# Performance work log

Measured on AMD Instinct MI355X. Metric: run time of the kernel, lower is better.

## Reference

```python
import jax, jax.numpy as jnp
import numpy as np

D_IN = 6      # raw node feature dim (self_attn_init first arg)
D_INIT = 16   # init encoding dim (self_attn_init second arg)
D_CAT = 22    # 6 + 16 (self_attn_enc first arg)
D_ENC = 64    # encoding dim (self_attn_enc second arg / gated_aggr_attn)
N = 1024      # number of nodes in node_cloud


def setup_inputs() -> dict:
    key = jax.random.key(0)
    ks = jax.random.split(key, 8)
    return {
        "node_cloud": jax.random.normal(ks[0], (N, D_IN), jnp.float32),
        "Wq_i": jax.random.normal(ks[1], (D_IN, D_INIT), jnp.float32) / np.sqrt(D_IN),
        "Wk_i": jax.random.normal(ks[2], (D_IN, D_INIT), jnp.float32) / np.sqrt(D_IN),
        "Wv_i": jax.random.normal(ks[3], (D_IN, D_INIT), jnp.float32) / np.sqrt(D_IN),
        "Wq_e": jax.random.normal(ks[4], (D_IN, D_ENC), jnp.float32) / np.sqrt(D_IN),
        "Wk_e": jax.random.normal(ks[5], (D_CAT, D_ENC), jnp.float32) / np.sqrt(D_CAT),
        "Wv_e": jax.random.normal(ks[6], (D_CAT, D_ENC), jnp.float32) / np.sqrt(D_CAT),
        "wg": jax.random.normal(ks[7], (D_ENC,), jnp.float32) / np.sqrt(D_ENC),
        "bg": jnp.zeros((), jnp.float32),
    }


def reference(node_cloud, Wq_i, Wk_i, Wv_i, Wq_e, Wk_e, Wv_e, wg, bg):
    # Stage 1: self_attn_init, batched over all C=N centres at once.
    # Per centre c: attend over every node, per-node 16-d encoding.
    Q_i = node_cloud @ Wq_i                     # [C, 16] (one query per centre)
    K_i = node_cloud @ Wk_i                     # [N, 16]
    V_i = node_cloud @ Wv_i                     # [N, 16]
    scores_i = (Q_i @ K_i.T) / np.sqrt(D_INIT)  # [C, N]
    a_i = jax.nn.softmax(scores_i, axis=-1)     # [C, N]
    nce_init = a_i[:, :, None] * V_i[None]      # [C, N, 16]

    # Stage 2: self_attn_enc on concat(raw node feats, init encodings).
    x = jnp.concatenate(
        [jnp.broadcast_to(node_cloud[None], (N, N, D_IN)), nce_init], axis=-1
    )                                            # [C, N, 22]
    Q_e = node_cloud @ Wq_e                      # [C, 64]
    K_e = jnp.einsum("cnf,fd->cnd", x, Wk_e)     # [C, N, 64]
    V_e = jnp.einsum("cnf,fd->cnd", x, Wv_e)     # [C, N, 64]
    scores_e = jnp.einsum("cnd,cd->cn", K_e, Q_e) / np.sqrt(D_ENC)  # [C, N]
    a_e = jax.nn.softmax(scores_e, axis=-1)      # [C, N]
    enc = a_e[:, :, None] * V_e                  # [C, N, 64]

    # Stage 3: gated_aggr_attn over the node axis -> one 64-vector per centre.
    g = jax.nn.sigmoid(enc @ wg + bg)            # [C, N]
    out = jnp.einsum("cn,cnd->cd", g, enc)       # [C, 64]
    return out
```

## Files before the change

kernel.cpp:

```cpp
#include <hip/hip_runtime.h>
#include <math.h>

#define NN 1024
#define DE 64
#define DCAT 22
#define GC 2
#define NTC 512
#define NWAVE (NTC/64)
#define NBLK (NN/GC)

#define OFF_XT   0
#define OFF_VIT  (OFF_XT + 6*NN)
#define OFF_GR   (OFF_VIT + 16*NN)
#define OFF_GV   (OFF_GR + NN)
#define OFF_QREC (OFF_GV + NN)

__device__ __forceinline__ float wave_sum(float v) {
    int t;
    t = __builtin_amdgcn_update_dpp(0, __float_as_int(v), 0x111, 0xf, 0xf, true); v += __int_as_float(t);
    t = __builtin_amdgcn_update_dpp(0, __float_as_int(v), 0x112, 0xf, 0xf, true); v += __int_as_float(t);
    t = __builtin_amdgcn_update_dpp(0, __float_as_int(v), 0x114, 0xf, 0xf, true); v += __int_as_float(t);
    t = __builtin_amdgcn_update_dpp(0, __float_as_int(v), 0x118, 0xf, 0xf, true); v += __int_as_float(t);
    t = __builtin_amdgcn_update_dpp(0, __float_as_int(v), 0x142, 0xf, 0xf, true); v += __int_as_float(t);
    t = __builtin_amdgcn_update_dpp(0, __float_as_int(v), 0x143, 0xf, 0xf, true); v += __int_as_float(t);
    return v;
}

__global__ __launch_bounds__(1024) void nce_setup(
    const float* __restrict__ nc,
    const float* __restrict__ Wq_i, const float* __restrict__ Wk_i,
    const float* __restrict__ Wv_i, const float* __restrict__ Wq_e,
    const float* __restrict__ Wk_e, const float* __restrict__ Wv_e,
    const float* __restrict__ wg, float* __restrict__ ws)
{
    __shared__ float s_wqi[96], s_wki[96], s_wvi[96];
    __shared__ float s_wqe[384], s_wke[1408], s_wve[1408], s_wg[64];
    __shared__ float s_M[6*DCAT], s_Mi[36], s_u[DCAT];
    const int tid = threadIdx.x;

    if (tid < 96) { s_wqi[tid]=Wq_i[tid]; s_wki[tid]=Wk_i[tid]; s_wvi[tid]=Wv_i[tid]; }
    { int t = tid - 128; if (t >= 0 && t < 384) s_wqe[t] = Wq_e[t]; }
    { int t = tid - 512; if (t >= 0 && t < 64)  s_wg[t]  = wg[t]; }
    for (int i = tid; i < 1408; i += 1024) { s_wke[i]=Wk_e[i]; s_wve[i]=Wv_e[i]; }
    __syncthreads();

    if (tid < 132) {
        const int f = tid % 6, k = tid / 6;
        float a = 0.f;
        #pragma unroll
        for (int d = 0; d < 64; ++d) a += s_wqe[f*64+d]*s_wke[k*64+d];
        s_M[f*DCAT+k] = a * 0.125f;
    } else if (tid < 168) {
        const int t = tid - 132, g = t % 6, f = t / 6;
        float a = 0.f;
        #pragma unroll
        for (int j = 0; j < 16; ++j) a += s_wqi[g*16+j]*s_wki[f*16+j];
        s_Mi[g*6+f] = a * 0.25f;
    } else if (tid < 190) {
        const int k = tid - 168;
        float a = 0.f;
        #pragma unroll
        for (int d = 0; d < 64; ++d) a += s_wve[k*64+d]*s_wg[d];
        s_u[k] = a;
    }
    __syncthreads();

    const int n = tid;
    float x[6];
    #pragma unroll
    for (int f = 0; f < 6; ++f) { x[f] = nc[n*6 + f]; ws[OFF_XT + f*NN + n] = x[f]; }

    float vi[16];
    #pragma unroll
    for (int j = 0; j < 16; ++j) {
        float a = 0.f;
        #pragma unroll
        for (int f = 0; f < 6; ++f) a += x[f]*s_wvi[f*16+j];
        vi[j] = a;
        ws[OFF_VIT + j*NN + n] = a;
    }
    float gr = 0.f, gv = 0.f;
    #pragma unroll
    for (int f = 0; f < 6; ++f)  gr += x[f]*s_u[f];
    #pragma unroll
    for (int j = 0; j < 16; ++j) gv += vi[j]*s_u[6+j];
    ws[OFF_GR + n] = gr;
    ws[OFF_GV + n] = gv;

    #pragma unroll
    for (int f = 0; f < 6; ++f) {
        float a = 0.f;
        #pragma unroll
        for (int g = 0; g < 6; ++g) a += x[g]*s_Mi[g*6+f];
        ws[OFF_QREC + f*NN + n] = a;
    }
    #pragma unroll
    for (int k = 0; k < DCAT; ++k) {
        float a = 0.f;
        #pragma unroll
        for (int f = 0; f < 6; ++f) a += x[f]*s_M[f*DCAT+k];
        ws[OFF_QREC + ((k < 6) ? (8+k) : (10+k))*NN + n] = a;
    }
}

__global__ __launch_bounds__(NTC, 4) void nce_centre(
    const float* __restrict__ ws, const float* __restrict__ bgp,
    const float* __restrict__ Wv_e, float* __restrict__ out)
{
    __shared__ float  s_wve[DCAT*DE];
    __shared__ float  s_q[GC][32];
    __shared__ float2 s_red1[NWAVE], s_red2[NWAVE];
    __shared__ float2 s_acc[NWAVE][DCAT];
    __shared__ float  s_fin[DCAT*GC];

    const int tid = threadIdx.x, wave = tid >> 6, lane = tid & 63;
    const int c0 = blockIdx.x*GC;

    for (int i = tid; i < DCAT*DE; i += NTC) s_wve[i] = Wv_e[i];
    if (tid < GC*32) s_q[tid >> 5][tid & 31] = ws[OFF_QREC + (tid & 31)*NN + c0 + (tid >> 5)];

    const int nA = tid, nB = tid + NTC;
    float xA[6], xB[6], viA[16], viB[16];
    #pragma unroll
    for (int f = 0; f < 6; ++f) { xA[f] = ws[OFF_XT + f*NN + nA]; xB[f] = ws[OFF_XT + f*NN + nB]; }
    #pragma unroll
    for (int j = 0; j < 16; ++j) { viA[j] = ws[OFF_VIT + j*NN + nA]; viB[j] = ws[OFF_VIT + j*NN + nB]; }
    const float grA = ws[OFF_GR + nA], grB = ws[OFF_GR + nB];
    const float gvA = ws[OFF_GV + nA], gvB = ws[OFF_GV + nB];
    const float bg = *bgp;
    __syncthreads();

    float aiA[GC], aiB[GC];
    #pragma unroll
    for (int c = 0; c < GC; ++c) {
        const float* q = s_q[c];
        float sA = 0.f, sB = 0.f;
        #pragma unroll
        for (int f = 0; f < 6; ++f) { sA += q[f]*xA[f]; sB += q[f]*xB[f]; }
        aiA[c] = __expf(sA); aiB[c] = __expf(sB);
    }
    {
        float r0 = wave_sum(aiA[0]+aiB[0]);
        float r1 = wave_sum(aiA[1]+aiB[1]);
        if (lane == 63) s_red1[wave] = make_float2(r0, r1);
    }
    __syncthreads();
    {
        float2 dd = s_red1[0];
        #pragma unroll
        for (int w2 = 1; w2 < NWAVE; ++w2) { float2 t = s_red1[w2]; dd.x += t.x; dd.y += t.y; }
        float inv0 = 1.f/dd.x, inv1 = 1.f/dd.y;
        aiA[0] *= inv0; aiB[0] *= inv0; aiA[1] *= inv1; aiB[1] *= inv1;
    }

    float w1A[GC], w2A[GC], w1B[GC], w2B[GC];
    {
        float eA[GC], eB[GC];
        #pragma unroll
        for (int c = 0; c < GC; ++c) {
            const float* q = s_q[c];
            float uA = 0.f, uB = 0.f, vA = 0.f, vB = 0.f;
            #pragma unroll
            for (int f = 0; f < 6; ++f) { uA += q[8+f]*xA[f]; uB += q[8+f]*xB[f]; }
            #pragma unroll
            for (int j = 0; j < 16; ++j) { vA += q[16+j]*viA[j]; vB += q[16+j]*viB[j]; }
            eA[c] = __expf(uA + aiA[c]*vA);
            eB[c] = __expf(uB + aiB[c]*vB);
        }
        float s0 = wave_sum(eA[0]+eB[0]);
        float s1 = wave_sum(eA[1]+eB[1]);
        if (lane == 63) s_red2[wave] = make_float2(s0, s1);
        __syncthreads();
        float2 dd = s_red2[0];
        #pragma unroll
        for (int w2 = 1; w2 < NWAVE; ++w2) { float2 t = s_red2[w2]; dd.x += t.x; dd.y += t.y; }
        float den[GC] = {dd.x, dd.y};
        #pragma unroll
        for (int c = 0; c < GC; ++c) {
            float inv = 1.f/den[c];
            float aeA = eA[c]*inv, aeB = eB[c]*inv;
            float preA = aeA*(grA + aiA[c]*gvA) + bg;
            float preB = aeB*(grB + aiB[c]*gvB) + bg;
            float gA = 1.f/(1.f + __expf(-preA));
            float gB = 1.f/(1.f + __expf(-preB));
            w1A[c] = gA*aeA; w2A[c] = w1A[c]*aiA[c];
            w1B[c] = gB*aeB; w2B[c] = w1B[c]*aiB[c];
        }
    }

    #pragma unroll
    for (int f = 0; f < 6; ++f) {
        float a0 = wave_sum(w1A[0]*xA[f] + w1B[0]*xB[f]);
        float a1 = wave_sum(w1A[1]*xA[f] + w1B[1]*xB[f]);
        if (lane == 63) s_acc[wave][f] = make_float2(a0, a1);
    }
    #pragma unroll
    for (int j = 0; j < 16; ++j) {
        float a0 = wave_sum(w2A[0]*viA[j] + w2B[0]*viB[j]);
        float a1 = wave_sum(w2A[1]*viA[j] + w2B[1]*viB[j]);
        if (lane == 63) s_acc[wave][6+j] = make_float2(a0, a1);
    }
    __syncthreads();
    if (tid < DCAT*GC) {
        const int k = tid >> 1, c = tid & 1;
        float a = 0.f;
        #pragma unroll
        for (int w2 = 0; w2 < NWAVE; ++w2)
            a += ((const float*)&s_acc[w2][k])[c];
        s_fin[k*GC + c] = a;
    }
    __syncthreads();

    if (tid < GC*DE) {
        const int c = tid >> 6, d = tid & 63;
        float o = 0.f;
        #pragma unroll
        for (int k = 0; k < DCAT; ++k) o += s_fin[k*GC + c]*s_wve[k*64 + d];
        out[(c0 + c)*DE + d] = o;
    }
}

extern "C" void kernel_launch(void* const* d_in, const int* in_sizes, int n_in,
                              void* d_out, int out_size, void* d_ws, size_t ws_size,
                              hipStream_t stream)
{
    const float* nc   = (const float*)d_in[0];
    const float* Wq_i = (const float*)d_in[1];
    const float* Wk_i = (const float*)d_in[2];
    const float* Wv_i = (const float*)d_in[3];
    const float* Wq_e = (const float*)d_in[4];
    const float* Wk_e = (const float*)d_in[5];
    const float* Wv_e = (const float*)d_in[6];
    const float* wg   = (const float*)d_in[7];
    const float* bg   = (const float*)d_in[8];
    float* out = (float*)d_out;
    float* ws  = (float*)d_ws;

    nce_setup<<<1, 1024, 0, stream>>>(nc, Wq_i, Wk_i, Wv_i, Wq_e, Wk_e, Wv_e, wg, ws);
    nce_centre<<<NBLK, NTC, 0, stream>>>(ws, bg, Wv_e, out);
}
```

Measured before the change: 21.38 us.

## Fuse setup kernel into per-centre kernel, recomputing per-node projections in each block

Merges the single-block setup kernel and the per-centre kernel into one launch. Each block now reloads the weights, recomputes the small folded matrices (M, Mi, u), the per-node V_i, gr and gv values, and its own centre queries, all directly from the inputs. This removes a kernel launch, the serial single-block setup phase, and the workspace round trip through global memory. In exchange it duplicates weight loads and small matmuls across all 512 blocks and raises shared-memory use per block.

```diff
diff --git a/kernel.cpp b/kernel.cpp
--- a/kernel.cpp
+++ b/kernel.cpp
@@ -8,12 +8,6 @@
 #define NTC 512
 #define NWAVE (NTC/64)
 #define NBLK (NN/GC)
-
-#define OFF_XT   0
-#define OFF_VIT  (OFF_XT + 6*NN)
-#define OFF_GR   (OFF_VIT + 16*NN)
-#define OFF_GV   (OFF_GR + NN)
-#define OFF_QREC (OFF_GV + NN)
 
 __device__ __forceinline__ float wave_sum(float v) {
     int t;
@@ -26,22 +20,34 @@
     return v;
 }
 
-__global__ __launch_bounds__(1024) void nce_setup(
+__global__ __launch_bounds__(NTC, 4) void nce_fused(
     const float* __restrict__ nc,
     const float* __restrict__ Wq_i, const float* __restrict__ Wk_i,
     const float* __restrict__ Wv_i, const float* __restrict__ Wq_e,
     const float* __restrict__ Wk_e, const float* __restrict__ Wv_e,
-    const float* __restrict__ wg, float* __restrict__ ws)
+    const float* __restrict__ wg,  const float* __restrict__ bgp,
+    float* __restrict__ out)
 {
-    __shared__ float s_wqi[96], s_wki[96], s_wvi[96];
-    __shared__ float s_wqe[384], s_wke[1408], s_wve[1408], s_wg[64];
-    __shared__ float s_M[6*DCAT], s_Mi[36], s_u[DCAT];
-    const int tid = threadIdx.x;
-
-    if (tid < 96) { s_wqi[tid]=Wq_i[tid]; s_wki[tid]=Wk_i[tid]; s_wvi[tid]=Wv_i[tid]; }
-    { int t = tid - 128; if (t >= 0 && t < 384) s_wqe[t] = Wq_e[t]; }
-    { int t = tid - 512; if (t >= 0 && t < 64)  s_wg[t]  = wg[t]; }
-    for (int i = tid; i < 1408; i += 1024) { s_wke[i]=Wk_e[i]; s_wve[i]=Wv_e[i]; }
+    __shared__ float  s_wqi[96], s_wki[96], s_wvi[96], s_wg[64];
+    __shared__ float  s_wqe[384], s_wke[1408], s_wve[1408];
+    __shared__ float  s_M[6*DCAT], s_Mi[36], s_u[DCAT];
+    __shared__ float  s_q[GC][32];
+    __shared__ float2 s_red1[NWAVE], s_red2[NWAVE];
+    __shared__ float2 s_acc[NWAVE][DCAT];
+    __shared__ float  s_fin[DCAT*GC];
+
+    const int tid  = threadIdx.x, wave = tid >> 6, lane = tid & 63;
+    const int c0   = blockIdx.x * GC;
+    const int nA   = tid, nB = tid + NTC;
+
+    float xA[6], xB[6];
+    #pragma unroll
+    for (int f = 0; f < 6; ++f) { xA[f] = nc[nA*6 + f]; xB[f] = nc[nB*6 + f]; }
+
+    if (tid < 96) { s_wqi[tid] = Wq_i[tid]; s_wki[tid] = Wk_i[tid]; s_wvi[tid] = Wv_i[tid]; }
+    else if (tid >= 128 && tid < 192) s_wg[tid-128] = wg[tid-128];
+    if (tid < 384) s_wqe[tid] = Wq_e[tid];
+    for (int i = tid; i < 1408; i += NTC) { s_wke[i] = Wk_e[i]; s_wve[i] = Wv_e[i]; }
     __syncthreads();
 
     if (tid < 132) {
@@ -65,68 +71,38 @@
     }
     __syncthreads();
 
-    const int n = tid;
-    float x[6];
-    #pragma unroll
-    for (int f = 0; f < 6; ++f) { x[f] = nc[n*6 + f]; ws[OFF_XT + f*NN + n] = x[f]; }
-
-    float vi[16];
+    float viA[16], viB[16];
     #pragma unroll
     for (int j = 0; j < 16; ++j) {
-        float a = 0.f;
-        #pragma unroll
-        for (int f = 0; f < 6; ++f) a += x[f]*s_wvi[f*16+j];
-        vi[j] = a;
-        ws[OFF_VIT + j*NN + n] = a;
-    }
-    float gr = 0.f, gv = 0.f;
-    #pragma unroll
-    for (int f = 0; f < 6; ++f)  gr += x[f]*s_u[f];
-    #pragma unroll
-    for (int j = 0; j < 16; ++j) gv += vi[j]*s_u[6+j];
-    ws[OFF_GR + n] = gr;
-    ws[OFF_GV + n] = gv;
-
-    #pragma unroll
-    for (int f = 0; f < 6; ++f) {
-        float a = 0.f;
-        #pragma unroll
-        for (int g = 0; g < 6; ++g) a += x[g]*s_Mi[g*6+f];
-        ws[OFF_QREC + f*NN + n] = a;
-    }
-    #pragma unroll
-    for (int k = 0; k < DCAT; ++k) {
-        float a = 0.f;
-        #pragma unroll
-        for (int f = 0; f < 6; ++f) a += x[f]*s_M[f*DCAT+k];
-        ws[OFF_QREC + ((k < 6) ? (8+k) : (10+k))*NN + n] = a;
-    }
-}
-
-__global__ __launch_bounds__(NTC, 4) void nce_centre(
-    const float* __restrict__ ws, const float* __restrict__ bgp,
-    const float* __restrict__ Wv_e, float* __restrict__ out)
-{
-    __shared__ float  s_wve[DCAT*DE];
-    __shared__ float  s_q[GC][32];
-    __shared__ float2 s_red1[NWAVE], s_red2[NWAVE];
-    __shared__ float2 s_acc[NWAVE][DCAT];
-    __shared__ float  s_fin[DCAT*GC];
-
-    const int tid = threadIdx.x, wave = tid >> 6, lane = tid & 63;
-    const int c0 = blockIdx.x*GC;
-
-    for (int i = tid; i < DCAT*DE; i += NTC) s_wve[i] = Wv_e[i];
-    if (tid < GC*32) s_q[tid >> 5][tid & 31] = ws[OFF_QREC + (tid & 31)*NN + c0 + (tid >> 5)];
-
-    const int nA = tid, nB = tid + NTC;
-    float xA[6], xB[6], viA[16], viB[16];
-    #pragma unroll
-    for (int f = 0; f < 6; ++f) { xA[f] = ws[OFF_XT + f*NN + nA]; xB[f] = ws[OFF_XT + f*NN + nB]; }
-    #pragma unroll
-    for (int j = 0; j < 16; ++j) { viA[j] = ws[OFF_VIT + j*NN + nA]; viB[j] = ws[OFF_VIT + j*NN + nB]; }
-    const float grA = ws[OFF_GR + nA], grB = ws[OFF_GR + nB];
-    const float gvA = ws[OFF_GV + nA], gvB = ws[OFF_GV + nB];
+        float a = 0.f, b = 0.f;
+        #pragma unroll
+        for (int f = 0; f < 6; ++f) { a += xA[f]*s_wvi[f*16+j]; b += xB[f]*s_wvi[f*16+j]; }
+        viA[j] = a; viB[j] = b;
+    }
+    float grA = 0.f, grB = 0.f, gvA = 0.f, gvB = 0.f;
+    #pragma unroll
+    for (int f = 0; f < 6; ++f)  { grA += xA[f]*s_u[f];    grB += xB[f]*s_u[f]; }
+    #pragma unroll
+    for (int j = 0; j < 16; ++j) { gvA += viA[j]*s_u[6+j]; gvB += viB[j]*s_u[6+j]; }
+
+    if (tid < GC*32) {
+        const int c = tid >> 5, k = tid & 31;
+        float xc[6];
+        #pragma unroll
+        for (int f = 0; f < 6; ++f) xc[f] = nc[(c0+c)*6 + f];
+        float a = 0.f;
+        if (k < 6) {
+            #pragma unroll
+            for (int g = 0; g < 6; ++g) a += xc[g]*s_Mi[g*6+k];
+        } else if (k >= 8 && k < 14) {
+            #pragma unroll
+            for (int f = 0; f < 6; ++f) a += xc[f]*s_M[f*DCAT + (k-8)];
+        } else if (k >= 16) {
+            #pragma unroll
+            for (int f = 0; f < 6; ++f) a += xc[f]*s_M[f*DCAT + 6 + (k-16)];
+        }
+        s_q[c][k] = a;
+    }
     const float bg = *bgp;
     __syncthreads();
 
@@ -234,8 +210,7 @@
     const float* wg   = (const float*)d_in[7];
     const float* bg   = (const float*)d_in[8];
     float* out = (float*)d_out;
-    float* ws  = (float*)d_ws;
-
-    nce_setup<<<1, 1024, 0, stream>>>(nc, Wq_i, Wk_i, Wv_i, Wq_e, Wk_e, Wv_e, wg, ws);
-    nce_centre<<<NBLK, NTC, 0, stream>>>(ws, bg, Wv_e, out);
+
+    nce_fused<<<NBLK, NTC, 0, stream>>>(nc, Wq_i, Wk_i, Wv_i, Wq_e, Wk_e, Wv_e,
+                                        wg, bg, out);
 }
```

Measured after the change: 21.63 us. About the same (+1.1%).
